# Kernel optimization log

Hardware: AMD Instinct MI355X
Metric: run time of the kernel (lower is better)

## Reference

```python
import jax, jax.numpy as jnp
import numpy as np
from jax import lax

THRESHOLDS = (0.25, 0.5, 0.75)
TAU = 100.0
NUM_CLASSES = 10
K = 32
RES_Z = 5.0
# each of the 16 binary logic gates is bilinear: g(a,b) = c0 + c1*a + c2*b + c3*a*b
GATE_COEF = jnp.array([
    [0, 0, 0, 0],   # 0: False
    [0, 0, 0, 1],   # 1: a AND b
    [0, 1, 0, -1],  # 2: a AND NOT b
    [0, 1, 0, 0],   # 3: a  (residual gate)
    [0, 0, 1, -1],  # 4: NOT a AND b
    [0, 0, 1, 0],   # 5: b
    [0, 1, 1, -2],  # 6: XOR
    [0, 1, 1, -1],  # 7: OR
    [1, -1, -1, 1], # 8: NOR
    [1, -1, -1, 2], # 9: XNOR
    [1, 0, -1, 0],  # 10: NOT b
    [1, 0, -1, 1],  # 11: a OR NOT b
    [1, -1, 0, 0],  # 12: NOT a
    [1, -1, 0, 1],  # 13: NOT a OR b
    [1, 0, 0, -1],  # 14: NAND
    [1, 0, 0, 0],   # 15: True
], dtype=jnp.float32)


def _gate_logits(key, shape):
    # residual init: pass-through gate (id 3) dominates
    w = 0.01 * jax.random.normal(key, shape, dtype=jnp.float32)
    return w.at[..., 3].add(RES_Z)


def _leaf_idx(rng, C, O, leaves=8, cpt=2, kk=9):
    # each tree uses cpt random input channels; each leaf picks one of them and a 3x3 position
    ch2 = rng.integers(0, C, size=(O, cpt))
    sel = rng.integers(0, cpt, size=(O, leaves))
    ch = np.take_along_axis(ch2, sel, axis=1)
    pos = rng.integers(0, kk, size=(O, leaves))
    return jnp.asarray(ch * kk + pos, dtype=jnp.int32)


def setup_inputs() -> dict:
    key = jax.random.key(0)
    ks = jax.random.split(key, 9)
    rng = np.random.default_rng(0)
    B = 128
    d = {"x": jax.random.uniform(ks[0], (B, 3, 32, 32), dtype=jnp.float32)}
    in_chs = [3 * len(THRESHOLDS), K, 4 * K, 16 * K]
    out_chs = [K, 4 * K, 16 * K, 32 * K]
    for i, (ci, co) in enumerate(zip(in_chs, out_chs)):
        d[f"c{i+1}_idx"] = _leaf_idx(rng, ci, co)
        d[f"c{i+1}_w"] = _gate_logits(ks[1 + i], (co, 7, 16))
    dims = [32 * K * 4, 1280 * K, 640 * K, 320 * K]
    for i in range(3):
        di, do = dims[i], dims[i + 1]
        d[f"l{i+1}_a"] = jnp.asarray(rng.integers(0, di, size=(do,)), dtype=jnp.int32)
        d[f"l{i+1}_b"] = jnp.asarray(rng.integers(0, di, size=(do,)), dtype=jnp.int32)
        d[f"l{i+1}_w"] = _gate_logits(ks[5 + i], (do, 16))
    return d


def _mix(logits):
    # softmax over 16 gates folded into 4 bilinear coefficients (fused gate mixture)
    return jax.nn.softmax(logits, axis=-1) @ GATE_COEF


def binarize(x):
    return jnp.concatenate([(x > t).astype(x.dtype) for t in THRESHOLDS], axis=1)


def tree_conv(x, leaf_idx, logits):
    # x: (B,C,H,W); leaf_idx: (O,8) into C*9 channel-major patch; logits: (O,7,16)
    B, C, H, W = x.shape
    xp = jnp.pad(x, ((0, 0), (0, 0), (1, 1), (1, 1)))
    patches = jnp.stack([xp[:, :, i:i + H, j:j + W] for i in range(3) for j in range(3)], axis=2)
    patches = patches.reshape(B, C * 9, H, W)
    vals = patches[:, leaf_idx]  # (B,O,8,H,W)
    m = _mix(logits)             # (O,7,4)
    node = 0
    for lvl in (4, 2, 1):
        a, b = vals[:, :, 0::2], vals[:, :, 1::2]
        w = m[:, node:node + lvl]  # (O,lvl,4)
        w0 = w[..., 0][None, :, :, None, None]
        w1 = w[..., 1][None, :, :, None, None]
        w2 = w[..., 2][None, :, :, None, None]
        w3 = w[..., 3][None, :, :, None, None]
        vals = w0 + w1 * a + w2 * b + w3 * (a * b)
        node += lvl
    return vals[:, :, 0]  # (B,O,H,W)


def or_pool(x):
    # OR of relaxed binary values == max pool 2x2/2
    return lax.reduce_window(x, -jnp.inf, lax.max, (1, 1, 2, 2), (1, 1, 2, 2), "VALID")


def logic_layer(x, a_idx, b_idx, logits):
    a = x[:, a_idx]  # (B,O)
    b = x[:, b_idx]
    w = _mix(logits)  # (O,4)
    return w[:, 0] + w[:, 1] * a + w[:, 2] * b + w[:, 3] * (a * b)


def group_sum(x):
    B = x.shape[0]
    return x.reshape(B, NUM_CLASSES, -1).sum(axis=-1) / TAU


def reference(x, c1_idx, c1_w, c2_idx, c2_w, c3_idx, c3_w, c4_idx, c4_w,
              l1_a, l1_b, l1_w, l2_a, l2_b, l2_w, l3_a, l3_b, l3_w):
    h = binarize(x)
    h = or_pool(tree_conv(h, c1_idx, c1_w))
    h = or_pool(tree_conv(h, c2_idx, c2_w))
    h = or_pool(tree_conv(h, c3_idx, c3_w))
    h = or_pool(tree_conv(h, c4_idx, c4_w))
    h = h.reshape(h.shape[0], -1)  # (B, 4096)
    h = logic_layer(h, l1_a, l1_b, l1_w)
    h = logic_layer(h, l2_a, l2_b, l2_w)
    h = logic_layer(h, l3_a, l3_b, l3_w)
    return group_sum(h)  # (B, 10)
```

## Files before the change

kernel.cpp:

```cpp
#include <hip/hip_runtime.h>
#include <hip/hip_fp16.h>

typedef float v2f __attribute__((ext_vector_type(2)));
typedef float v4f __attribute__((ext_vector_type(4)));
typedef int   v4i __attribute__((ext_vector_type(4)));

__device__ __constant__ float GC[16][4] = {
  {0,0,0,0},{0,0,0,1},{0,1,0,-1},{0,1,0,0},
  {0,0,1,-1},{0,0,1,0},{0,1,1,-2},{0,1,1,-1},
  {1,-1,-1,1},{1,-1,-1,2},{1,0,-1,0},{1,0,-1,1},
  {1,-1,0,0},{1,-1,0,1},{1,0,0,-1},{1,0,0,0}};

__device__ __forceinline__ v2f pk_mul(v2f a, v2f b) {
  v2f d;
  asm("v_pk_mul_f32 %0, %1, %2" : "=v"(d) : "v"(a), "v"(b));
  return d;
}
__device__ __forceinline__ v2f gate2pk(v2f a, v2f b, v2f w01, v2f w23) {
  v2f t = pk_mul(a, b);
  v2f d;
  asm("v_pk_fma_f32 %0, %1, %2, %2 op_sel:[0,1,0] op_sel_hi:[1,1,0]"
      : "=v"(d) : "v"(a), "v"(w01));
  asm("v_pk_fma_f32 %0, %1, %2, %0 op_sel:[0,0,0] op_sel_hi:[1,0,1]"
      : "+v"(d) : "v"(b), "v"(w23));
  asm("v_pk_fma_f32 %0, %1, %2, %0 op_sel:[0,1,0] op_sel_hi:[1,1,1]"
      : "+v"(d) : "v"(t), "v"(w23));
  return d;
}

__device__ __forceinline__ void mix_one(const float* lp, float* op) {
  float e[16];
  float s = 0.f;
  #pragma unroll
  for (int i = 0; i < 16; ++i) { e[i] = __expf(lp[i]); s += e[i]; }
  float inv = 1.0f / s;
  float w0 = 0.f, w1 = 0.f, w2 = 0.f, w3 = 0.f;
  #pragma unroll
  for (int i = 0; i < 16; ++i) {
    float p = e[i] * inv;
    w0 = fmaf(p, GC[i][0], w0);
    w1 = fmaf(p, GC[i][1], w1);
    w2 = fmaf(p, GC[i][2], w2);
    w3 = fmaf(p, GC[i][3], w3);
  }
  op[0] = w0; op[1] = w1; op[2] = w2; op[3] = w3;
}

struct PrepArgs {
  const float* logits[7];
  float* outm[7];
  const int* cidx[4];
  int* offt[4];
};

__global__ __launch_bounds__(256) void prep_k(PrepArgs A) {
  int gid = blockIdx.x * 256 + threadIdx.x;
  if (gid < 83552) {
    const int n[7] = {224, 896, 3584, 7168, 40960, 20480, 10240};
    int g = gid, seg = 0;
    while (seg < 6 && g >= n[seg]) { g -= n[seg]; ++seg; }
    mix_one(A.logits[seg] + (size_t)g * 16, A.outm[seg] + (size_t)g * 4);
  } else if (gid < 85248) {
    int r = gid - 83552;
    int L, rr, H;
    if (r < 32)       { L = 0; rr = r;       H = 32; }
    else if (r < 160) { L = 1; rr = r - 32;  H = 16; }
    else if (r < 672) { L = 2; rr = r - 160; H = 8;  }
    else              { L = 3; rr = r - 672; H = 4;  }
    const int* ci = A.cidx[L] + rr * 8;
    int* oo = A.offt[L] + rr * 8;
    int W2 = H + 2;
    #pragma unroll
    for (int l = 0; l < 8; ++l) {
      int idx = ci[l];
      int c  = idx / 9;
      int k  = idx - 9 * c;
      int di = k / 3 - 1;
      int dj = k - 3 * (k / 3) - 1;
      oo[l] = (c * (H + 2) + 1 + di) * W2 + 1 + dj;
    }
  }
}

struct MegaArgs {
  const float* x;
  const float* mc[4];
  const int*   offt[4];
  const int*   la[3];
  const int*   lb[3];
  const float* mlw[3];
  float* out;
};

extern __shared__ char S[];

template<int OH, int OW, int LOGOW, int IW2, int PIXCNT, int LOGPIX,
         int NCH, int ITERS, bool UNI, bool HALO>
__device__ __forceinline__ void conv_stage(
    const float* in, float* outb,
    const int* __restrict__ offt, const float* __restrict__ mtab, int tid) {
  int pix = tid & (PIXCNT - 1);
  int ch0 = tid >> LOGPIX;
  int pw  = pix & (OW - 1);
  int ph  = pix >> LOGOW;
  int pixbase = (2 * ph) * IW2 + 2 * pw;
  #pragma unroll 2
  for (int it = 0; it < ITERS; ++it) {
    int ch = ch0 + NCH * it;
    if (UNI) ch = __builtin_amdgcn_readfirstlane(ch);
    const int* ot = offt + ch * 8;
    const float* mt = mtab + ch * 28;
    v4f g0 = *(const v4f*)(mt +  0);
    v4f g1 = *(const v4f*)(mt +  4);
    v4f g2 = *(const v4f*)(mt +  8);
    v4f g3 = *(const v4f*)(mt + 12);
    v4f g4 = *(const v4f*)(mt + 16);
    v4f g5 = *(const v4f*)(mt + 20);
    v4f g6 = *(const v4f*)(mt + 24);
    v2f v01[8], v23[8];
    #pragma unroll
    for (int l = 0; l < 8; ++l) {
      int a0 = ot[l] + pixbase;
      v2f t0; t0.x = in[a0];       t0.y = in[a0 + 1];
      v2f t1; t1.x = in[a0 + IW2]; t1.y = in[a0 + IW2 + 1];
      v01[l] = t0; v23[l] = t1;
    }
    v2f u0 = gate2pk(v01[0], v01[1], g0.xy, g0.zw);
    v2f u1 = gate2pk(v01[2], v01[3], g1.xy, g1.zw);
    v2f u2 = gate2pk(v01[4], v01[5], g2.xy, g2.zw);
    v2f u3 = gate2pk(v01[6], v01[7], g3.xy, g3.zw);
    v2f s0 = gate2pk(u0, u1, g4.xy, g4.zw);
    v2f s1 = gate2pk(u2, u3, g5.xy, g5.zw);
    v2f r0 = gate2pk(s0, s1, g6.xy, g6.zw);
    u0 = gate2pk(v23[0], v23[1], g0.xy, g0.zw);
    u1 = gate2pk(v23[2], v23[3], g1.xy, g1.zw);
    u2 = gate2pk(v23[4], v23[5], g2.xy, g2.zw);
    u3 = gate2pk(v23[6], v23[7], g3.xy, g3.zw);
    s0 = gate2pk(u0, u1, g4.xy, g4.zw);
    s1 = gate2pk(u2, u3, g5.xy, g5.zw);
    v2f r1 = gate2pk(s0, s1, g6.xy, g6.zw);
    float res = fmaxf(fmaxf(r0.x, r0.y), fmaxf(r1.x, r1.y));
    if (HALO)
      outb[ch * (OH + 2) * (OW + 2) + (1 + ph) * (OW + 2) + 1 + pw] = res;
    else
      outb[ch * (OH * OW) + pix] = res;
  }
}

__global__ __launch_bounds__(512, 2) void mega_k(MegaArgs A) {
  int tid = threadIdx.x;
  int b = blockIdx.x;
  float* binb = (float*)(S);
  float* buf1 = (float*)(S + 53248);
  float* buf2 = (float*)(S);
  float* buf3 = (float*)(S + 53248);
  float* h4   = (float*)(S);
  __half* g1h = (__half*)(S + 16384);
  __half* g2h = (__half*)(S + 98304);
  float* lsum = (float*)(S + 139264);

  for (int i = tid; i < 10404; i += 512) binb[i] = 0.f;
  if (tid < 10) lsum[tid] = 0.f;
  __syncthreads();
  const float* xb = A.x + (size_t)b * 3072;
  #pragma unroll
  for (int i = 0; i < 6; ++i) {
    int idx = tid + 512 * i;
    float v = xb[idx];
    int rgb = idx >> 10;
    int rem = idx & 1023;
    int y = rem >> 5, xx = rem & 31;
    int base = (1 + y) * 34 + 1 + xx;
    binb[(0 + rgb) * 1156 + base] = v > 0.25f ? 1.f : 0.f;
    binb[(3 + rgb) * 1156 + base] = v > 0.50f ? 1.f : 0.f;
    binb[(6 + rgb) * 1156 + base] = v > 0.75f ? 1.f : 0.f;
  }
  __syncthreads();

  for (int i = tid; i < 10368; i += 512) buf1[i] = 0.f;
  __syncthreads();
  conv_stage<16,16,4,34,256,8,2,16,true,true>(binb, buf1, A.offt[0], A.mc[0], tid);
  __syncthreads();
  for (int i = tid; i < 12800; i += 512) buf2[i] = 0.f;
  __syncthreads();
  conv_stage<8,8,3,18,64,6,8,16,true,true>(buf1, buf2, A.offt[1], A.mc[1], tid);
  __syncthreads();
  for (int i = tid; i < 18432; i += 512) buf3[i] = 0.f;
  __syncthreads();
  conv_stage<4,4,2,10,16,4,32,16,false,true>(buf2, buf3, A.offt[2], A.mc[2], tid);
  __syncthreads();
  conv_stage<2,2,1,6,4,2,128,8,false,false>(buf3, h4, A.offt[3], A.mc[3], tid);
  __syncthreads();

  {
    const v4i* a4 = (const v4i*)A.la[0];
    const v4i* b4 = (const v4i*)A.lb[0];
    const v4f* w4 = (const v4f*)A.mlw[0];
    #pragma unroll 2
    for (int g = 0; g < 20; ++g) {
      int q = tid + 512 * g;
      v4i ai = a4[q], bi = b4[q];
      #pragma unroll
      for (int i = 0; i < 4; ++i) {
        v4f w = w4[4 * q + i];
        float a = h4[ai[i]], bb = h4[bi[i]];
        g1h[4 * q + i] = __float2half(fmaf(w.w, a * bb, fmaf(w.z, bb, fmaf(w.y, a, w.x))));
      }
    }
  }
  __syncthreads();
  {
    const v4i* a4 = (const v4i*)A.la[1];
    const v4i* b4 = (const v4i*)A.lb[1];
    const v4f* w4 = (const v4f*)A.mlw[1];
    #pragma unroll 2
    for (int g = 0; g < 10; ++g) {
      int q = tid + 512 * g;
      v4i ai = a4[q], bi = b4[q];
      #pragma unroll
      for (int i = 0; i < 4; ++i) {
        v4f w = w4[4 * q + i];
        float a = __half2float(g1h[ai[i]]), bb = __half2float(g2h == 0 ? g1h[bi[i]] : g1h[bi[i]]);
        g2h[4 * q + i] = __float2half(fmaf(w.w, a * bb, fmaf(w.z, bb, fmaf(w.y, a, w.x))));
      }
    }
  }
  __syncthreads();
  {
    const v4i* a4 = (const v4i*)A.la[2];
    const v4i* b4 = (const v4i*)A.lb[2];
    const v4f* w4 = (const v4f*)A.mlw[2];
    int wv = tid >> 6, lane = tid & 63;
    #pragma unroll
    for (int g = 0; g < 5; ++g) {
      int q = tid + 512 * g;
      v4i ai = a4[q], bi = b4[q];
      float s = 0.f;
      #pragma unroll
      for (int i = 0; i < 4; ++i) {
        v4f w = w4[4 * q + i];
        float a = __half2float(g2h[ai[i]]), bb = __half2float(g2h[bi[i]]);
        s += fmaf(w.w, a * bb, fmaf(w.z, bb, fmaf(w.y, a, w.x)));
      }
      #pragma unroll
      for (int m = 1; m < 64; m <<= 1) s += __shfl_xor(s, m);
      if (lane == 0) atomicAdd(&lsum[(wv + 8 * g) >> 2], s);
    }
  }
  __syncthreads();
  if (tid < 10) A.out[b * 10 + tid] = lsum[tid] * 0.01f;
}

extern "C" void kernel_launch(void* const* d_in, const int* in_sizes, int n_in,
                              void* d_out, int out_size, void* d_ws, size_t ws_size,
                              hipStream_t stream) {
  const float* x   = (const float*)d_in[0];
  const int*   c1i = (const int*)d_in[1];
  const float* c1w = (const float*)d_in[2];
  const int*   c2i = (const int*)d_in[3];
  const float* c2w = (const float*)d_in[4];
  const int*   c3i = (const int*)d_in[5];
  const float* c3w = (const float*)d_in[6];
  const int*   c4i = (const int*)d_in[7];
  const float* c4w = (const float*)d_in[8];
  const int*   l1a = (const int*)d_in[9];
  const int*   l1b = (const int*)d_in[10];
  const float* l1w = (const float*)d_in[11];
  const int*   l2a = (const int*)d_in[12];
  const int*   l2b = (const int*)d_in[13];
  const float* l2w = (const float*)d_in[14];
  const int*   l3a = (const int*)d_in[15];
  const int*   l3b = (const int*)d_in[16];
  const float* l3w = (const float*)d_in[17];

  float* ws = (float*)d_ws;
  float* mc1 = ws;
  float* mc2 = mc1 + 896;
  float* mc3 = mc2 + 3584;
  float* mc4 = mc3 + 14336;
  float* ml1 = mc4 + 28672;
  float* ml2 = ml1 + 163840;
  float* ml3 = ml2 + 81920;
  int* off1 = (int*)(ml3 + 40960);
  int* off2 = off1 + 256;
  int* off3 = off2 + 1024;
  int* off4 = off3 + 4096;

  PrepArgs P;
  P.logits[0] = c1w; P.outm[0] = mc1;
  P.logits[1] = c2w; P.outm[1] = mc2;
  P.logits[2] = c3w; P.outm[2] = mc3;
  P.logits[3] = c4w; P.outm[3] = mc4;
  P.logits[4] = l1w; P.outm[4] = ml1;
  P.logits[5] = l2w; P.outm[5] = ml2;
  P.logits[6] = l3w; P.outm[6] = ml3;
  P.cidx[0] = c1i; P.offt[0] = off1;
  P.cidx[1] = c2i; P.offt[1] = off2;
  P.cidx[2] = c3i; P.offt[2] = off3;
  P.cidx[3] = c4i; P.offt[3] = off4;
  prep_k<<<333, 256, 0, stream>>>(P);

  MegaArgs M;
  M.x = x;
  M.mc[0] = mc1; M.mc[1] = mc2; M.mc[2] = mc3; M.mc[3] = mc4;
  M.offt[0] = off1; M.offt[1] = off2; M.offt[2] = off3; M.offt[3] = off4;
  M.la[0] = l1a; M.lb[0] = l1b; M.mlw[0] = ml1;
  M.la[1] = l2a; M.lb[1] = l2b; M.mlw[1] = ml2;
  M.la[2] = l3a; M.lb[2] = l3b; M.mlw[2] = ml3;
  M.out = (float*)d_out;

  static bool attr_set = false;
  if (!attr_set) {
    hipFuncSetAttribute((const void*)mega_k,
                        hipFuncAttributeMaxDynamicSharedMemorySize, 139328);
    attr_set = true;
  }
  mega_k<<<128, 512, 139328, stream>>>(M);
}
```

Measured before the change: 161.1 us.

## Pad and swizzle conv LDS layouts and double block size to 1024 threads

Changes the shared-memory feature-map layout to use odd row pitches plus a per-row-pair shift (encoded in high bits of the precomputed offsets) to reduce LDS bank conflicts in the tree-conv gathers. The block size is also doubled to 1024 threads, with per-stage channel/iteration counts and logic-layer loops rebalanced to match. Only 128 blocks run, so more threads per block is meant to raise per-CU parallelism. The cost is extra address arithmetic per leaf load and higher register pressure under the 1024-thread launch bound.

```diff
diff --git a/kernel.cpp b/kernel.cpp
--- a/kernel.cpp
+++ b/kernel.cpp
@@ -62,14 +62,17 @@
     mix_one(A.logits[seg] + (size_t)g * 16, A.outm[seg] + (size_t)g * 4);
   } else if (gid < 85248) {
     int r = gid - 83552;
-    int L, rr, H;
-    if (r < 32)       { L = 0; rr = r;       H = 32; }
-    else if (r < 160) { L = 1; rr = r - 32;  H = 16; }
-    else if (r < 672) { L = 2; rr = r - 160; H = 8;  }
-    else              { L = 3; rr = r - 672; H = 4;  }
+    int L, rr;
+    if (r < 32)       { L = 0; rr = r;       }
+    else if (r < 160) { L = 1; rr = r - 32;  }
+    else if (r < 672) { L = 2; rr = r - 160; }
+    else              { L = 3; rr = r - 672; }
+    const int W2Pt[4] = {35, 19, 11, 6};
+    const int CSt[4]  = {1190, 342, 110, 36};
+    const int swzt[4] = {1, 1, 1, 0};
+    int W2P = W2Pt[L], CS = CSt[L], swz = swzt[L];
     const int* ci = A.cidx[L] + rr * 8;
     int* oo = A.offt[L] + rr * 8;
-    int W2 = H + 2;
     #pragma unroll
     for (int l = 0; l < 8; ++l) {
       int idx = ci[l];
@@ -77,7 +80,11 @@
       int k  = idx - 9 * c;
       int di = k / 3 - 1;
       int dj = k - 3 * (k / 3) - 1;
-      oo[l] = (c * (H + 2) + 1 + di) * W2 + 1 + dj;
+      int yl = 1 + di;
+      int off = c * CS + yl * W2P + 1 + dj;
+      if (swz)
+        off |= (((yl >> 1) & 1) << 28) | ((((yl + 1) >> 1) & 1) << 29);
+      oo[l] = off;
     }
   }
 }
@@ -94,8 +101,8 @@
 
 extern __shared__ char S[];
 
-template<int OH, int OW, int LOGOW, int IW2, int PIXCNT, int LOGPIX,
-         int NCH, int ITERS, bool UNI, bool HALO>
+template<int OH, int OW, int LOGOW, int IW2P, int PIXCNT, int LOGPIX,
+         int NCH, int ITERS, bool UNI, bool RSWZ, bool OHALO, int OW2P, bool OSWZ>
 __device__ __forceinline__ void conv_stage(
     const float* in, float* outb,
     const int* __restrict__ offt, const float* __restrict__ mtab, int tid) {
@@ -103,7 +110,8 @@
   int ch0 = tid >> LOGPIX;
   int pw  = pix & (OW - 1);
   int ph  = pix >> LOGOW;
-  int pixbase = (2 * ph) * IW2 + 2 * pw;
+  int pixbase = 2 * ph * IW2P + 2 * pw;
+  int ph1 = ph & 1;
   #pragma unroll 2
   for (int it = 0; it < ITERS; ++it) {
     int ch = ch0 + NCH * it;
@@ -120,9 +128,18 @@
     v2f v01[8], v23[8];
     #pragma unroll
     for (int l = 0; l < 8; ++l) {
-      int a0 = ot[l] + pixbase;
-      v2f t0; t0.x = in[a0];       t0.y = in[a0 + 1];
-      v2f t1; t1.x = in[a0 + IW2]; t1.y = in[a0 + IW2 + 1];
+      int e = ot[l];
+      int at, ab;
+      if (RSWZ) {
+        int off = e & 0x0FFFFFFF;
+        at = off + pixbase + ((ph1 ^ (e >> 28)) & 1);
+        ab = off + pixbase + IW2P + ((ph1 ^ (e >> 29)) & 1);
+      } else {
+        at = e + pixbase;
+        ab = at + IW2P;
+      }
+      v2f t0; t0.x = in[at]; t0.y = in[at + 1];
+      v2f t1; t1.x = in[ab]; t1.y = in[ab + 1];
       v01[l] = t0; v23[l] = t1;
     }
     v2f u0 = gate2pk(v01[0], v01[1], g0.xy, g0.zw);
@@ -140,56 +157,65 @@
     s1 = gate2pk(u2, u3, g5.xy, g5.zw);
     v2f r1 = gate2pk(s0, s1, g6.xy, g6.zw);
     float res = fmaxf(fmaxf(r0.x, r0.y), fmaxf(r1.x, r1.y));
-    if (HALO)
-      outb[ch * (OH + 2) * (OW + 2) + (1 + ph) * (OW + 2) + 1 + pw] = res;
-    else
+    if (OHALO) {
+      int oy = 1 + ph;
+      int widx = ch * ((OH + 2) * OW2P) + oy * OW2P + 1 + pw;
+      if (OSWZ) widx += (oy >> 1) & 1;
+      outb[widx] = res;
+    } else {
       outb[ch * (OH * OW) + pix] = res;
-  }
-}
-
-__global__ __launch_bounds__(512, 2) void mega_k(MegaArgs A) {
+    }
+  }
+}
+
+__global__ __launch_bounds__(1024) void mega_k(MegaArgs A) {
   int tid = threadIdx.x;
   int b = blockIdx.x;
   float* binb = (float*)(S);
-  float* buf1 = (float*)(S + 53248);
+  float* buf1 = (float*)(S + 56320);
   float* buf2 = (float*)(S);
-  float* buf3 = (float*)(S + 53248);
+  float* buf3 = (float*)(S + 56320);
   float* h4   = (float*)(S);
   __half* g1h = (__half*)(S + 16384);
   __half* g2h = (__half*)(S + 98304);
   float* lsum = (float*)(S + 139264);
 
-  for (int i = tid; i < 10404; i += 512) binb[i] = 0.f;
+  for (int i = tid; i < 10710; i += 1024) binb[i] = 0.f;
   if (tid < 10) lsum[tid] = 0.f;
   __syncthreads();
   const float* xb = A.x + (size_t)b * 3072;
   #pragma unroll
-  for (int i = 0; i < 6; ++i) {
-    int idx = tid + 512 * i;
+  for (int i = 0; i < 3; ++i) {
+    int idx = tid + 1024 * i;
     float v = xb[idx];
     int rgb = idx >> 10;
     int rem = idx & 1023;
     int y = rem >> 5, xx = rem & 31;
-    int base = (1 + y) * 34 + 1 + xx;
-    binb[(0 + rgb) * 1156 + base] = v > 0.25f ? 1.f : 0.f;
-    binb[(3 + rgb) * 1156 + base] = v > 0.50f ? 1.f : 0.f;
-    binb[(6 + rgb) * 1156 + base] = v > 0.75f ? 1.f : 0.f;
-  }
-  __syncthreads();
-
-  for (int i = tid; i < 10368; i += 512) buf1[i] = 0.f;
-  __syncthreads();
-  conv_stage<16,16,4,34,256,8,2,16,true,true>(binb, buf1, A.offt[0], A.mc[0], tid);
-  __syncthreads();
-  for (int i = tid; i < 12800; i += 512) buf2[i] = 0.f;
-  __syncthreads();
-  conv_stage<8,8,3,18,64,6,8,16,true,true>(buf1, buf2, A.offt[1], A.mc[1], tid);
-  __syncthreads();
-  for (int i = tid; i < 18432; i += 512) buf3[i] = 0.f;
-  __syncthreads();
-  conv_stage<4,4,2,10,16,4,32,16,false,true>(buf2, buf3, A.offt[2], A.mc[2], tid);
-  __syncthreads();
-  conv_stage<2,2,1,6,4,2,128,8,false,false>(buf3, h4, A.offt[3], A.mc[3], tid);
+    int oy = 1 + y;
+    int base = oy * 35 + 1 + xx + ((oy >> 1) & 1);
+    binb[(0 + rgb) * 1190 + base] = v > 0.25f ? 1.f : 0.f;
+    binb[(3 + rgb) * 1190 + base] = v > 0.50f ? 1.f : 0.f;
+    binb[(6 + rgb) * 1190 + base] = v > 0.75f ? 1.f : 0.f;
+  }
+  __syncthreads();
+
+  for (int i = tid; i < 10944; i += 1024) buf1[i] = 0.f;
+  __syncthreads();
+  conv_stage<16,16,4, 35, 256,8, 4, 8, true, true, true, 19, true>(
+      binb, buf1, A.offt[0], A.mc[0], tid);
+  __syncthreads();
+  for (int i = tid; i < 14080; i += 1024) buf2[i] = 0.f;
+  __syncthreads();
+  conv_stage<8,8,3, 19, 64,6, 16, 8, true, true, true, 11, true>(
+      buf1, buf2, A.offt[1], A.mc[1], tid);
+  __syncthreads();
+  for (int i = tid; i < 18432; i += 1024) buf3[i] = 0.f;
+  __syncthreads();
+  conv_stage<4,4,2, 11, 16,4, 64, 8, false, true, true, 6, false>(
+      buf2, buf3, A.offt[2], A.mc[2], tid);
+  __syncthreads();
+  conv_stage<2,2,1, 6, 4,2, 256, 4, false, false, false, 1, false>(
+      buf3, h4, A.offt[3], A.mc[3], tid);
   __syncthreads();
 
   {
@@ -197,8 +223,8 @@
     const v4i* b4 = (const v4i*)A.lb[0];
     const v4f* w4 = (const v4f*)A.mlw[0];
     #pragma unroll 2
-    for (int g = 0; g < 20; ++g) {
-      int q = tid + 512 * g;
+    for (int g = 0; g < 10; ++g) {
+      int q = tid + 1024 * g;
       v4i ai = a4[q], bi = b4[q];
       #pragma unroll
       for (int i = 0; i < 4; ++i) {
@@ -214,13 +240,13 @@
     const v4i* b4 = (const v4i*)A.lb[1];
     const v4f* w4 = (const v4f*)A.mlw[1];
     #pragma unroll 2
-    for (int g = 0; g < 10; ++g) {
-      int q = tid + 512 * g;
+    for (int g = 0; g < 5; ++g) {
+      int q = tid + 1024 * g;
       v4i ai = a4[q], bi = b4[q];
       #pragma unroll
       for (int i = 0; i < 4; ++i) {
         v4f w = w4[4 * q + i];
-        float a = __half2float(g1h[ai[i]]), bb = __half2float(g2h == 0 ? g1h[bi[i]] : g1h[bi[i]]);
+        float a = __half2float(g1h[ai[i]]), bb = __half2float(g1h[bi[i]]);
         g2h[4 * q + i] = __float2half(fmaf(w.w, a * bb, fmaf(w.z, bb, fmaf(w.y, a, w.x))));
       }
     }
@@ -230,21 +256,23 @@
     const v4i* a4 = (const v4i*)A.la[2];
     const v4i* b4 = (const v4i*)A.lb[2];
     const v4f* w4 = (const v4f*)A.mlw[2];
-    int wv = tid >> 6, lane = tid & 63;
+    int lane = tid & 63;
     #pragma unroll
-    for (int g = 0; g < 5; ++g) {
-      int q = tid + 512 * g;
-      v4i ai = a4[q], bi = b4[q];
-      float s = 0.f;
-      #pragma unroll
-      for (int i = 0; i < 4; ++i) {
-        v4f w = w4[4 * q + i];
-        float a = __half2float(g2h[ai[i]]), bb = __half2float(g2h[bi[i]]);
-        s += fmaf(w.w, a * bb, fmaf(w.z, bb, fmaf(w.y, a, w.x)));
+    for (int g = 0; g < 3; ++g) {
+      int q = tid + 1024 * g;
+      if (q < 2560) {
+        v4i ai = a4[q], bi = b4[q];
+        float s = 0.f;
+        #pragma unroll
+        for (int i = 0; i < 4; ++i) {
+          v4f w = w4[4 * q + i];
+          float a = __half2float(g2h[ai[i]]), bb = __half2float(g2h[bi[i]]);
+          s += fmaf(w.w, a * bb, fmaf(w.z, bb, fmaf(w.y, a, w.x)));
+        }
+        #pragma unroll
+        for (int m = 1; m < 64; m <<= 1) s += __shfl_xor(s, m);
+        if (lane == 0) atomicAdd(&lsum[q >> 8], s);
       }
-      #pragma unroll
-      for (int m = 1; m < 64; m <<= 1) s += __shfl_xor(s, m);
-      if (lane == 0) atomicAdd(&lsum[(wv + 8 * g) >> 2], s);
     }
   }
   __syncthreads();
@@ -315,5 +343,5 @@
                         hipFuncAttributeMaxDynamicSharedMemorySize, 139328);
     attr_set = true;
   }
-  mega_k<<<128, 512, 139328, stream>>>(M);
-}
+  mega_k<<<128, 1024, 139328, stream>>>(M);
+}
```

Result: faster. 157.4 us (-2.3%).
